# Optimization experiments

Hardware: AMD Instinct MI355X
Metric: run time of the kernel (lower is better)

Reference implementation:

```python
import jax, jax.numpy as jnp
import numpy as np

DIA = 2  # dilation of the 3x3 shift pattern


def setup_inputs() -> dict:
    key = jax.random.key(0)
    ks = jax.random.split(key, 6)
    B, C, H, W = 8, 3, 512, 512
    return {
        "x": jax.random.normal(ks[0], (B, C, H, W), dtype=jnp.float32),
        "y": jax.random.normal(ks[1], (B, C, 2 * H, 2 * W), dtype=jnp.float32),
        "w1": jax.random.normal(ks[2], (C,), dtype=jnp.float32) * 0.1,
        "b1": jax.random.normal(ks[3], (C,), dtype=jnp.float32) * 0.1,
        "w2": jax.random.normal(ks[4], (C,), dtype=jnp.float32) * 0.1,
        "b2": jax.random.normal(ks[5], (C,), dtype=jnp.float32) * 0.1,
    }


def _per_channel(x, w, b):
    # grouped 1x1 conv with groups == channels == per-channel scale + bias
    return x * w[None, :, None, None] + b[None, :, None, None]


def reference(x, y, w1, b1, w2, b2):
    D = DIA
    h, w = x.shape[2], x.shape[3]
    # conv1 is applied twice to the same input -> x_o == x_r
    x_o = jax.nn.relu(_per_channel(x, w1, b1))
    x_r = x_o
    # 9-way shifted zero-padded sum == dilated 3x3 box-sum
    pad = jnp.pad(x_o, ((0, 0), (0, 0), (D, D), (D, D)))
    out_n = jnp.zeros_like(x_o)
    for i in range(3):
        for j in range(3):
            out_n = out_n + pad[:, :, i * D:i * D + h, j * D:j * D + w]
    gate = jax.nn.sigmoid(_per_channel(out_n, w2, b2))
    out = gate * x_r
    # F.interpolate default mode='nearest': src = floor(dst * in / out)
    H2, W2 = y.shape[2], y.shape[3]
    ih = (jnp.arange(H2) * h) // H2
    iw = (jnp.arange(W2) * w) // W2
    up = out[:, :, ih, :][:, :, :, iw]
    return y + up
```

## Files before the change

kernel.cpp:

```cpp
#include <hip/hip_runtime.h>


#define DIA 2

__global__ __launch_bounds__(256) void fused_kernel(
    const float* __restrict__ x, const float* __restrict__ y,
    const float* __restrict__ w1v, const float* __restrict__ b1v,
    const float* __restrict__ w2v, const float* __restrict__ b2v,
    float* __restrict__ out)
{
    constexpr int C = 3, H = 512, W = 512, W2 = 1024;

    int idx = blockIdx.x * blockDim.x + threadIdx.x;
    int wp = idx & (W / 2 - 1);
    int h  = __builtin_amdgcn_readfirstlane((idx >> 8) & (H - 1));
    int bc = __builtin_amdgcn_readfirstlane(idx >> 17);
    int c  = bc % C;
    int w0 = wp * 2;

    const float s_w1 = w1v[c], s_b1 = b1v[c];
    const float s_w2 = w2v[c], s_b2 = b2v[c];

    const float* __restrict__ xrow = x + ((size_t)bc * H + (size_t)h) * W;

    const bool ok0 = (h >= DIA), ok2 = (h < H - DIA);
    const bool lok = (w0 > 0), rok = (w0 + 2 < W);
    const float m0 = ok0 ? 1.f : 0.f;
    const float m2 = ok2 ? 1.f : 0.f;
    const float mL = lok ? 1.f : 0.f;
    const float mR = rok ? 1.f : 0.f;

    const float* r1 = xrow;
    const float* r0 = ok0 ? (xrow - DIA * W) : xrow;
    const float* r2 = ok2 ? (xrow + DIA * W) : xrow;
    const int wl = lok ? (w0 - 2) : w0;
    const int wr = rok ? (w0 + 2) : w0;

    float2 L0 = *(const float2*)(r0 + wl);
    float2 M0 = *(const float2*)(r0 + w0);
    float2 R0 = *(const float2*)(r0 + wr);
    float2 L1 = *(const float2*)(r1 + wl);
    float2 M1 = *(const float2*)(r1 + w0);
    float2 R1 = *(const float2*)(r1 + wr);
    float2 L2 = *(const float2*)(r2 + wl);
    float2 M2 = *(const float2*)(r2 + w0);
    float2 R2 = *(const float2*)(r2 + wr);

    size_t obase = (((size_t)bc * (2 * H) + (size_t)(2 * h)) * W2) + (size_t)(2 * w0);
    float4 ya = *(const float4*)(y + obase);
    float4 yb = *(const float4*)(y + obase + W2);

    auto act = [&](float v) { return fmaxf(fmaf(v, s_w1, s_b1), 0.f); };

    float xo0 = act(M1.x);
    float xo1 = act(M1.y);

    float sum0 = mL * act(L1.x) + xo0 + mR * act(R1.x);
    float sum1 = mL * act(L1.y) + xo1 + mR * act(R1.y);
    sum0 += m0 * (mL * act(L0.x) + act(M0.x) + mR * act(R0.x));
    sum1 += m0 * (mL * act(L0.y) + act(M0.y) + mR * act(R0.y));
    sum0 += m2 * (mL * act(L2.x) + act(M2.x) + mR * act(R2.x));
    sum1 += m2 * (mL * act(L2.y) + act(M2.y) + mR * act(R2.y));

    float z0 = fmaf(sum0, s_w2, s_b2);
    float z1 = fmaf(sum1, s_w2, s_b2);
    float o0 = xo0 / (1.f + __expf(-z0));
    float o1 = xo1 / (1.f + __expf(-z1));

    *(float4*)(out + obase)      = make_float4(ya.x + o0, ya.y + o0, ya.z + o1, ya.w + o1);
    *(float4*)(out + obase + W2) = make_float4(yb.x + o0, yb.y + o0, yb.z + o1, yb.w + o1);
}

extern "C" void kernel_launch(void* const* d_in, const int* in_sizes, int n_in,
                              void* d_out, int out_size, void* d_ws, size_t ws_size,
                              hipStream_t stream) {
    const float* x  = (const float*)d_in[0];
    const float* y  = (const float*)d_in[1];
    const float* w1 = (const float*)d_in[2];
    const float* b1 = (const float*)d_in[3];
    const float* w2 = (const float*)d_in[4];
    const float* b2 = (const float*)d_in[5];
    float* out = (float*)d_out;

    constexpr int B = 8, C = 3, H = 512, W = 512;
    int total_threads = B * C * H * (W / 2);
    int block = 256;
    int grid  = total_threads / block;
    fused_kernel<<<grid, block, 0, stream>>>(x, y, w1, b1, w2, b2, out);
}
```

Baseline: 199.4 us.

## Process four rows per block with software-pipelined loads and XCD-aware block swizzle

Each block now handles four consecutive output rows instead of one. Loads for the next row are issued before the current row is computed, and inline-asm register pins keep the compiler from sinking those loads, so memory latency overlaps with compute. Block indices are remapped so each group of eight consecutive blocks spreads across chunks, meant to give each XCD a contiguous region for L2 reuse of the overlapping stencil rows. The cost is higher register pressure and a grid that is four times smaller, which lowers occupancy and parallelism.

```diff
diff --git a/kernel.cpp b/kernel.cpp
--- a/kernel.cpp
+++ b/kernel.cpp
@@ -2,6 +2,20 @@
 
 
 #define DIA 2
+
+struct Stage {
+    float2 L0, M0, R0, L1, M1, R1, L2, M2, R2;
+    float4 ya, yb;
+};
+
+#define PIN(s) asm volatile("" :: \
+    "v"((s).L0.x), "v"((s).L0.y), "v"((s).M0.x), "v"((s).M0.y), \
+    "v"((s).R0.x), "v"((s).R0.y), "v"((s).L1.x), "v"((s).L1.y), \
+    "v"((s).M1.x), "v"((s).M1.y), "v"((s).R1.x), "v"((s).R1.y), \
+    "v"((s).L2.x), "v"((s).L2.y), "v"((s).M2.x), "v"((s).M2.y), \
+    "v"((s).R2.x), "v"((s).R2.y), \
+    "v"((s).ya.x), "v"((s).ya.y), "v"((s).ya.z), "v"((s).ya.w), \
+    "v"((s).yb.x), "v"((s).yb.y), "v"((s).yb.z), "v"((s).yb.w))
 
 __global__ __launch_bounds__(256) void fused_kernel(
     const float* __restrict__ x, const float* __restrict__ y,
@@ -10,65 +24,81 @@
     float* __restrict__ out)
 {
     constexpr int C = 3, H = 512, W = 512, W2 = 1024;
+    constexpr int NBLK = 3072, CHUNK = NBLK / 8;
 
-    int idx = blockIdx.x * blockDim.x + threadIdx.x;
-    int wp = idx & (W / 2 - 1);
-    int h  = __builtin_amdgcn_readfirstlane((idx >> 8) & (H - 1));
-    int bc = __builtin_amdgcn_readfirstlane(idx >> 17);
-    int c  = bc % C;
-    int w0 = wp * 2;
+    int g = blockIdx.x;
+    int p = (g & 7) * CHUNK + (g >> 3);
+
+    int row0 = p * 4;
+    int bc   = row0 >> 9;
+    int h0   = row0 & (H - 1);
+    int c    = bc % C;
+    int w0   = threadIdx.x * 2;
 
     const float s_w1 = w1v[c], s_b1 = b1v[c];
     const float s_w2 = w2v[c], s_b2 = b2v[c];
 
-    const float* __restrict__ xrow = x + ((size_t)bc * H + (size_t)h) * W;
-
-    const bool ok0 = (h >= DIA), ok2 = (h < H - DIA);
     const bool lok = (w0 > 0), rok = (w0 + 2 < W);
-    const float m0 = ok0 ? 1.f : 0.f;
-    const float m2 = ok2 ? 1.f : 0.f;
     const float mL = lok ? 1.f : 0.f;
     const float mR = rok ? 1.f : 0.f;
-
-    const float* r1 = xrow;
-    const float* r0 = ok0 ? (xrow - DIA * W) : xrow;
-    const float* r2 = ok2 ? (xrow + DIA * W) : xrow;
     const int wl = lok ? (w0 - 2) : w0;
     const int wr = rok ? (w0 + 2) : w0;
 
-    float2 L0 = *(const float2*)(r0 + wl);
-    float2 M0 = *(const float2*)(r0 + w0);
-    float2 R0 = *(const float2*)(r0 + wr);
-    float2 L1 = *(const float2*)(r1 + wl);
-    float2 M1 = *(const float2*)(r1 + w0);
-    float2 R1 = *(const float2*)(r1 + wr);
-    float2 L2 = *(const float2*)(r2 + wl);
-    float2 M2 = *(const float2*)(r2 + w0);
-    float2 R2 = *(const float2*)(r2 + wr);
+    const float* __restrict__ ximg = x + (size_t)bc * H * W;
 
-    size_t obase = (((size_t)bc * (2 * H) + (size_t)(2 * h)) * W2) + (size_t)(2 * w0);
-    float4 ya = *(const float4*)(y + obase);
-    float4 yb = *(const float4*)(y + obase + W2);
+    auto load_stage = [&](int h) -> Stage {
+        const float* r1 = ximg + (size_t)h * W;
+        const float* r0 = (h >= DIA)     ? (r1 - DIA * W) : r1;
+        const float* r2 = (h < H - DIA)  ? (r1 + DIA * W) : r1;
+        Stage s;
+        s.L0 = *(const float2*)(r0 + wl);
+        s.M0 = *(const float2*)(r0 + w0);
+        s.R0 = *(const float2*)(r0 + wr);
+        s.L1 = *(const float2*)(r1 + wl);
+        s.M1 = *(const float2*)(r1 + w0);
+        s.R1 = *(const float2*)(r1 + wr);
+        s.L2 = *(const float2*)(r2 + wl);
+        s.M2 = *(const float2*)(r2 + w0);
+        s.R2 = *(const float2*)(r2 + wr);
+        size_t ob = (((size_t)bc * (2 * H) + (size_t)(2 * h)) * W2) + (size_t)(2 * w0);
+        s.ya = *(const float4*)(y + ob);
+        s.yb = *(const float4*)(y + ob + W2);
+        return s;
+    };
 
     auto act = [&](float v) { return fmaxf(fmaf(v, s_w1, s_b1), 0.f); };
 
-    float xo0 = act(M1.x);
-    float xo1 = act(M1.y);
+    auto compute_store = [&](const Stage& s, int h) {
+        const float m0 = (h >= DIA)    ? 1.f : 0.f;
+        const float m2 = (h < H - DIA) ? 1.f : 0.f;
+        float xo0 = act(s.M1.x);
+        float xo1 = act(s.M1.y);
+        float sum0 = mL * act(s.L1.x) + xo0 + mR * act(s.R1.x);
+        float sum1 = mL * act(s.L1.y) + xo1 + mR * act(s.R1.y);
+        sum0 += m0 * (mL * act(s.L0.x) + act(s.M0.x) + mR * act(s.R0.x));
+        sum1 += m0 * (mL * act(s.L0.y) + act(s.M0.y) + mR * act(s.R0.y));
+        sum0 += m2 * (mL * act(s.L2.x) + act(s.M2.x) + mR * act(s.R2.x));
+        sum1 += m2 * (mL * act(s.L2.y) + act(s.M2.y) + mR * act(s.R2.y));
+        float z0 = fmaf(sum0, s_w2, s_b2);
+        float z1 = fmaf(sum1, s_w2, s_b2);
+        float o0 = xo0 / (1.f + __expf(-z0));
+        float o1 = xo1 / (1.f + __expf(-z1));
+        size_t ob = (((size_t)bc * (2 * H) + (size_t)(2 * h)) * W2) + (size_t)(2 * w0);
+        *(float4*)(out + ob)      = make_float4(s.ya.x + o0, s.ya.y + o0, s.ya.z + o1, s.ya.w + o1);
+        *(float4*)(out + ob + W2) = make_float4(s.yb.x + o0, s.yb.y + o0, s.yb.z + o1, s.yb.w + o1);
+    };
 
-    float sum0 = mL * act(L1.x) + xo0 + mR * act(R1.x);
-    float sum1 = mL * act(L1.y) + xo1 + mR * act(R1.y);
-    sum0 += m0 * (mL * act(L0.x) + act(M0.x) + mR * act(R0.x));
-    sum1 += m0 * (mL * act(L0.y) + act(M0.y) + mR * act(R0.y));
-    sum0 += m2 * (mL * act(L2.x) + act(M2.x) + mR * act(R2.x));
-    sum1 += m2 * (mL * act(L2.y) + act(M2.y) + mR * act(R2.y));
-
-    float z0 = fmaf(sum0, s_w2, s_b2);
-    float z1 = fmaf(sum1, s_w2, s_b2);
-    float o0 = xo0 / (1.f + __expf(-z0));
-    float o1 = xo1 / (1.f + __expf(-z1));
-
-    *(float4*)(out + obase)      = make_float4(ya.x + o0, ya.y + o0, ya.z + o1, ya.w + o1);
-    *(float4*)(out + obase + W2) = make_float4(yb.x + o0, yb.y + o0, yb.z + o1, yb.w + o1);
+    Stage s0 = load_stage(h0 + 0);
+    Stage s1 = load_stage(h0 + 1);
+    PIN(s1);
+    compute_store(s0, h0 + 0);
+    Stage s2 = load_stage(h0 + 2);
+    PIN(s2);
+    compute_store(s1, h0 + 1);
+    Stage s3 = load_stage(h0 + 3);
+    PIN(s3);
+    compute_store(s2, h0 + 2);
+    compute_store(s3, h0 + 3);
 }
 
 extern "C" void kernel_launch(void* const* d_in, const int* in_sizes, int n_in,
@@ -82,9 +112,6 @@
     const float* b2 = (const float*)d_in[5];
     float* out = (float*)d_out;
 
-    constexpr int B = 8, C = 3, H = 512, W = 512;
-    int total_threads = B * C * H * (W / 2);
-    int block = 256;
-    int grid  = total_threads / block;
+    int grid = 3072, block = 256;
     fused_kernel<<<grid, block, 0, stream>>>(x, y, w1, b1, w2, b2, out);
 }
```

Measured after the change: 222.9 us. 1.12x slower.
